# Performance work log

Measured on AMD Instinct MI355X. Metric: run time of the kernel, lower is better.

The kernel has to match this reference:

```python
import jax, jax.numpy as jnp
import numpy as np

B, T, C, H = 4, 2048, 1024, 16
HD = C // H


def setup_inputs() -> dict:
    key = jax.random.key(0)
    ks = jax.random.split(key, 9)
    s = 1.0 / np.sqrt(C)
    return {
        "x": jax.random.normal(ks[0], (B, T, C), dtype=jnp.float32),
        "Wk": jax.random.uniform(ks[1], (C, C), jnp.float32, -s, s),
        "bk": jax.random.uniform(ks[2], (C,), jnp.float32, -s, s),
        "Wq": jax.random.uniform(ks[3], (C, C), jnp.float32, -s, s),
        "bq": jax.random.uniform(ks[4], (C,), jnp.float32, -s, s),
        "Wv": jax.random.uniform(ks[5], (C, C), jnp.float32, -s, s),
        "bv": jax.random.uniform(ks[6], (C,), jnp.float32, -s, s),
        "Wp": jax.random.uniform(ks[7], (C, C), jnp.float32, -s, s),
        "bp": jax.random.uniform(ks[8], (C,), jnp.float32, -s, s),
        "padding_mask": jnp.ones((B, T), dtype=jnp.int32),
    }


def reference(x, Wk, bk, Wq, bq, Wv, bv, Wp, bp, padding_mask):
    # torch nn.Linear: y = x @ W.T + b  (W is [out, in])
    def split_heads(t):  # [B,T,C] -> [B,H,T,HD]
        return t.reshape(B, T, H, HD).transpose(0, 2, 1, 3)

    k = split_heads(x @ Wk.T + bk)
    q = split_heads(x @ Wq.T + bq)
    v = split_heads(x @ Wv.T + bv)

    scale = 1.0 / jnp.sqrt(jnp.float32(HD))
    att = jnp.einsum("bhqd,bhkd->bhqk", q, k) * scale  # [B,H,T,T]

    causal = jnp.tril(jnp.ones((T, T), dtype=bool))  # [T,T]
    pad = (padding_mask != 0)[:, None, None, :]       # [B,1,1,T]
    mask = causal[None, None, :, :] & pad
    att = jnp.where(mask, att, -jnp.inf)
    att = jax.nn.softmax(att, axis=-1)

    y = jnp.einsum("bhqk,bhkd->bhqd", att, v)  # [B,H,T,HD]
    y = y.transpose(0, 2, 1, 3).reshape(B, T, C)
    return y @ Wp.T + bp
```

## Files before the change

kernel.cpp:

```cpp
#include <hip/hip_runtime.h>
#include <hip/hip_bf16.h>
#include <math.h>
#include <stdint.h>

#define BB 4
#define TT 2048
#define CC 1024
#define HH 16
#define HD 64
#define MM (BB*TT)
#define NQT2 16
#define SCQ 0.180336878f

using f32x2  = __attribute__((ext_vector_type(2))) float;
using f32x4  = __attribute__((ext_vector_type(4))) float;
using f32x16 = __attribute__((ext_vector_type(16))) float;
using i32x4  = __attribute__((ext_vector_type(4))) int;
using bf16x4 = __attribute__((ext_vector_type(4))) __bf16;
using bf16x8 = __attribute__((ext_vector_type(8))) __bf16;

__device__ __forceinline__ float fast_exp2(float x) {
  return __builtin_amdgcn_exp2f(x);
}

__device__ __forceinline__ int cvt_pk_bf16(float lo, float hi_) {
  int r;
  asm("v_cvt_pk_bf16_f32 %0, %1, %2" : "=v"(r) : "v"(lo), "v"(hi_));
  return r;
}

__device__ __forceinline__ f32x2 max2(f32x2 a, f32x2 b) {
  return __builtin_elementwise_max(a, b);
}

__device__ __forceinline__ void gload_lds16(const void* g, void* l) {
  __builtin_amdgcn_global_load_lds(
      (__attribute__((address_space(1))) void*)(void*)(g),
      (__attribute__((address_space(3))) void*)(l), 16, 0, 0);
}

__global__ __launch_bounds__(256)
void cvt_f32_bf16(const float* __restrict__ s, __bf16* __restrict__ d, int n4) {
  int i = blockIdx.x * 256 + threadIdx.x;
  if (i >= n4) return;
  float4 v = ((const float4*)s)[i];
  bf16x4 o;
  o[0] = (__bf16)v.x; o[1] = (__bf16)v.y; o[2] = (__bf16)v.z; o[3] = (__bf16)v.w;
  *(bf16x4*)(d + (size_t)i * 4) = o;
}

__global__ __launch_bounds__(256)
void cvt_w4(const float* __restrict__ Wq, const float* __restrict__ Wk,
            const float* __restrict__ Wv, const float* __restrict__ Wp,
            __bf16* __restrict__ wqkv, __bf16* __restrict__ wpb) {
  int which = blockIdx.y;
  const float* s = which == 0 ? Wq : which == 1 ? Wk : which == 2 ? Wv : Wp;
  __bf16* d = which == 3 ? wpb : wqkv + (size_t)which * CC * CC;
  float sc = which == 0 ? SCQ : 1.f;
  int i = blockIdx.x * 256 + threadIdx.x;
  float4 v = ((const float4*)s)[i];
  bf16x4 o;
  o[0] = (__bf16)(v.x * sc); o[1] = (__bf16)(v.y * sc);
  o[2] = (__bf16)(v.z * sc); o[3] = (__bf16)(v.w * sc);
  *(bf16x4*)(d + (size_t)i * 4) = o;
}

#define WAITV4 asm volatile("s_waitcnt vmcnt(4)" ::: "memory")
#define WAITV0 asm volatile("s_waitcnt vmcnt(0)" ::: "memory")
#define BARR   __builtin_amdgcn_s_barrier()
#define SB0    __builtin_amdgcn_sched_barrier(0)

__global__ __launch_bounds__(256, 2)
void gemm_qkv(const __bf16* __restrict__ A, const __bf16* __restrict__ Bm,
              const float* __restrict__ b0, const float* __restrict__ b1,
              const float* __restrict__ b2, __bf16* __restrict__ out,
              __bf16* __restrict__ vt) {
  __shared__ __bf16 U[24576];
  char* Ub = (char*)U;
  const int tid = threadIdx.x;
  const int wid = tid >> 6, lane = tid & 63;
  const int g = lane >> 4, lq = lane & 15;
  const int bx0 = blockIdx.x;
  const int bx = (bx0 & 7) * 192 + (bx0 >> 3);
  const int bm = bx / 24, bn = bx % 24;
  const int brow = bm << 7, bcol = bn << 7;
  const int wr = (wid >> 1) << 6, wc = (wid & 1) << 6;

  const int c0 = tid, c1 = tid + 256;
  const int r0 = c0 >> 2, s0_ = (((c0 & 3) - (r0 >> 1)) & 3) << 4;
  const int r1 = c1 >> 2, s1_ = (((c1 & 3) - (r1 >> 1)) & 3) << 4;
  const char* Ag = (const char*)A;
  const char* Bg = (const char*)Bm;

#define STAGEQ(ko, buf)                                                       \
  {                                                                           \
    gload_lds16(Ag + (size_t)(brow + r0) * 2048 + (ko) + s0_,                 \
                Ub + (buf) * 8192 + c0 * 16);                                 \
    gload_lds16(Ag + (size_t)(brow + r1) * 2048 + (ko) + s1_,                 \
                Ub + (buf) * 8192 + c1 * 16);                                 \
    gload_lds16(Bg + (size_t)(bcol + r0) * 2048 + (ko) + s0_,                 \
                Ub + 24576 + (buf) * 8192 + c0 * 16);                         \
    gload_lds16(Bg + (size_t)(bcol + r1) * 2048 + (ko) + s1_,                 \
                Ub + 24576 + (buf) * 8192 + c1 * 16);                         \
  }

  f32x4 acc[4][4] = {};

  STAGEQ(0, 0); STAGEQ(64, 1);
  int cur = 0;
#pragma unroll 1
  for (int t = 0; t < 32; ++t) {
    if (t + 1 < 32) { WAITV4; } else { WAITV0; }
    BARR; SB0;
    if (t + 2 < 32) {
      int nb = cur + 2; if (nb >= 3) nb -= 3;
      STAGEQ((t + 2) << 6, nb);
    }
    const char* Ac = Ub + cur * 8192;
    const char* Bc = Ub + 24576 + cur * 8192;
    bf16x8 av[4], bv[4];
#pragma unroll
    for (int m = 0; m < 4; ++m) {
      int row = wr + m * 16 + lq;
      int sl = (g + (row >> 1)) & 3;
      av[m] = *(const bf16x8*)(Ac + row * 64 + sl * 16);
    }
#pragma unroll
    for (int n = 0; n < 4; ++n) {
      int row = wc + n * 16 + lq;
      int sl = (g + (row >> 1)) & 3;
      bv[n] = *(const bf16x8*)(Bc + row * 64 + sl * 16);
    }
#pragma unroll
    for (int m = 0; m < 4; ++m)
#pragma unroll
      for (int n = 0; n < 4; ++n)
        acc[m][n] = __builtin_amdgcn_mfma_f32_16x16x32_bf16(av[m], bv[n], acc[m][n], 0, 0, 0);
    SB0;
    cur = (cur == 2) ? 0 : cur + 1;
  }
#undef STAGEQ

  const int proj = bn >> 3;
  if (proj < 2) {
    const float* bias = proj == 0 ? b0 : b1;
    const float bsc = proj == 0 ? SCQ : 1.f;
#pragma unroll
    for (int n = 0; n < 4; ++n) {
      int col = bcol + wc + n * 16 + lq;
      int cw = col & (CC - 1);
      float bb = bias[cw] * bsc;
      int h_ = cw >> 6, d_ = cw & (HD - 1);
#pragma unroll
      for (int m = 0; m < 4; ++m) {
        int row0 = brow + wr + m * 16 + g * 4;
#pragma unroll
        for (int i = 0; i < 4; ++i) {
          int row = row0 + i;
          int b_ = row >> 11, t_ = row & (TT - 1);
          out[((size_t)proj << 23) +
              ((((size_t)b_ * HH + h_) * TT + t_) << 6) + d_] =
              (__bf16)(acc[m][n][i] + bb);
        }
      }
    }
  } else {
    __syncthreads();
    __bf16* lt = U;
    const int cv0 = (bn & 7) << 7;
    const int b_ = brow >> 11, t0 = brow & (TT - 1);
    const int hbase = (bn & 7) << 1;
    const int rd_d = tid >> 2, rd_tb = (tid & 3) << 5;
#pragma unroll
    for (int cc = 0; cc < 2; ++cc) {
      if ((wid & 1) == cc) {
#pragma unroll
        for (int n = 0; n < 4; ++n) {
          int c = (n << 4) + lq;
          float bb = b2[cv0 + (cc << 6) + c];
#pragma unroll
          for (int m = 0; m < 4; ++m) {
            int r = wr + (m << 4) + (g << 2);
            bf16x4 pk;
#pragma unroll
            for (int i = 0; i < 4; ++i)
              pk[i] = (__bf16)(acc[m][n][i] + bb);
            *(bf16x4*)(lt + c * 130 + r) = pk;
          }
        }
      }
      __syncthreads();
      __bf16* dst = vt + (((size_t)((b_ * HH + hbase + cc) * HD + rd_d)) << 11)
                       + t0 + rd_tb;
      const __bf16* srcl = lt + rd_d * 130 + rd_tb;
#pragma unroll
      for (int j = 0; j < 4; ++j)
        *(bf16x8*)(dst + j * 8) = *(const bf16x8*)(srcl + j * 8);
      __syncthreads();
    }
  }
}

__global__ __launch_bounds__(256, 2)
void gemm_proj(const __bf16* __restrict__ A, const __bf16* __restrict__ Bm,
               const float* __restrict__ bias, float* __restrict__ out) {
  __shared__ __bf16 U[24576];
  char* Ub = (char*)U;
  const int tid = threadIdx.x;
  const int wid = tid >> 6, lane = tid & 63;
  const int g = lane >> 4, lq = lane & 15;
  const int bx0 = blockIdx.x;
  const int bx = (bx0 & 7) * 64 + (bx0 >> 3);
  const int brow = (bx >> 3) << 7;
  const int bcol = (bx & 7) << 7;
  const int wr = (wid >> 1) << 6, wc = (wid & 1) << 6;

  const int c0 = tid, c1 = tid + 256;
  const int r0 = c0 >> 2, s0_ = (((c0 & 3) - (r0 >> 1)) & 3) << 4;
  const int r1 = c1 >> 2, s1_ = (((c1 & 3) - (r1 >> 1)) & 3) << 4;
  const char* Ag = (const char*)A;
  const char* Bg = (const char*)Bm;

#define STAGEP(ko, buf)                                                       \
  {                                                                           \
    gload_lds16(Ag + (size_t)(brow + r0) * 2048 + (ko) + s0_,                 \
                Ub + (buf) * 8192 + c0 * 16);                                 \
    gload_lds16(Ag + (size_t)(brow + r1) * 2048 + (ko) + s1_,                 \
                Ub + (buf) * 8192 + c1 * 16);                                 \
    gload_lds16(Bg + (size_t)(bcol + r0) * 2048 + (ko) + s0_,                 \
                Ub + 24576 + (buf) * 8192 + c0 * 16);                         \
    gload_lds16(Bg + (size_t)(bcol + r1) * 2048 + (ko) + s1_,                 \
                Ub + 24576 + (buf) * 8192 + c1 * 16);                         \
  }

  f32x4 acc[4][4] = {};

  STAGEP(0, 0); STAGEP(64, 1);
  int cur = 0;
#pragma unroll 1
  for (int t = 0; t < 32; ++t) {
    if (t + 1 < 32) { WAITV4; } else { WAITV0; }
    BARR; SB0;
    if (t + 2 < 32) {
      int nb = cur + 2; if (nb >= 3) nb -= 3;
      STAGEP((t + 2) << 6, nb);
    }
    const char* Ac = Ub + cur * 8192;
    const char* Bc = Ub + 24576 + cur * 8192;
    bf16x8 av[4], bv[4];
#pragma unroll
    for (int m = 0; m < 4; ++m) {
      int row = wr + m * 16 + lq;
      int sl = (g + (row >> 1)) & 3;
      av[m] = *(const bf16x8*)(Ac + row * 64 + sl * 16);
    }
#pragma unroll
    for (int n = 0; n < 4; ++n) {
      int row = wc + n * 16 + lq;
      int sl = (g + (row >> 1)) & 3;
      bv[n] = *(const bf16x8*)(Bc + row * 64 + sl * 16);
    }
#pragma unroll
    for (int m = 0; m < 4; ++m)
#pragma unroll
      for (int n = 0; n < 4; ++n)
        acc[m][n] = __builtin_amdgcn_mfma_f32_16x16x32_bf16(av[m], bv[n], acc[m][n], 0, 0, 0);
    SB0;
    cur = (cur == 2) ? 0 : cur + 1;
  }
#undef STAGEP

#pragma unroll
  for (int m = 0; m < 4; ++m) {
#pragma unroll
    for (int n = 0; n < 4; ++n) {
      int col = bcol + wc + n * 16 + lq;
      float bb = bias[col];
      int row0 = brow + wr + m * 16 + g * 4;
#pragma unroll
      for (int i = 0; i < 4; ++i)
        out[(size_t)(row0 + i) * CC + col] = acc[m][n][i] + bb;
    }
  }
}

__global__ __launch_bounds__(256, 4)
void attn_fwd(const __bf16* __restrict__ Q, const __bf16* __restrict__ K,
              const __bf16* __restrict__ Vt, const int* __restrict__ pm,
              __bf16* __restrict__ Y) {
  __shared__ __bf16 Ks[2][64 * 64];
  __shared__ __bf16 Vs[2][64 * 64];
  __shared__ int flg;
  const int tid = threadIdx.x, wid = tid >> 6, lane = tid & 63;
  const int l31 = lane & 31, hi = lane >> 5;
  const int bx = blockIdx.x;
  const int bh = bx & 63, jj = bx >> 6;
  const int qi = 15 - (4 * (jj >> 2) + ((jj + (jj >> 2)) & 3));
  const int b_ = bh >> 4, h_ = bh & 15;
  const __bf16* Qb = Q + (size_t)bh * TT * HD;
  const __bf16* Kb = K + (size_t)bh * TT * HD;
  const __bf16* Vb = Vt + (size_t)bh * HD * TT;
  const int* pmb = pm + b_ * TT;

  const int so = tid * 16;
  const int srow = tid >> 3;
  const int scol = (so & 127) ^ ((srow & 7) << 4);

  const int q0 = qi << 7;
  const int qw = q0 + wid * 32;
  const int ntiles = 2 * qi + 2;
  const int sw0 = (l31 & 7) << 4;

  bf16x8 qf[4];
#pragma unroll
  for (int s = 0; s < 4; ++s)
    qf[s] = *(const bf16x8*)(Qb + (size_t)(qw + l31) * HD + s * 16 + hi * 8);
  SB0;

  int4 pa4 = ((const int4*)pmb)[tid];
  int4 pb4 = ((const int4*)pmb)[tid + 256];
  bool okp = pa4.x && pa4.y && pa4.z && pa4.w &&
             pb4.x && pb4.y && pb4.z && pb4.w;
  if (tid == 0) flg = 1;
  __syncthreads();
  if (!okp) flg = 0;

  {
    char* kd = (char*)&Ks[0][0] + so;
    char* vd = (char*)&Vs[0][0] + so;
#pragma unroll
    for (int j = 0; j < 2; ++j) {
      gload_lds16((const char*)Kb + (size_t)(srow + 32 * j) * 128 + scol,
                  kd + j * 4096);
      gload_lds16((const char*)Vb + (size_t)(srow + 32 * j) * (TT * 2) + scol,
                  vd + j * 4096);
    }
  }
  __syncthreads();
  const bool allones = (flg != 0);

  f32x16 o0 = {}, o1 = {};
  f32x16 vzero = {};
  float lsum = 0.f;
  float m = -INFINITY;

  int cur = 0;
#pragma unroll 1
  for (int t = 0; t < ntiles; ++t) {
    const int kv0 = t << 6;
    WAITV0;
    __builtin_amdgcn_s_barrier(); SB0;
    if (t + 1 < ntiles) {
      char* kd = (char*)&Ks[0][0] + (cur ^ 1) * 8192 + so;
      char* vd = (char*)&Vs[0][0] + (cur ^ 1) * 8192 + so;
      const size_t nk = (size_t)(kv0 + 64);
#pragma unroll
      for (int j = 0; j < 2; ++j) {
        gload_lds16((const char*)Kb + (nk + srow + 32 * j) * 128 + scol,
                    kd + j * 4096);
        gload_lds16((const char*)Vb + (size_t)(srow + 32 * j) * (TT * 2) +
                        nk * 2 + scol,
                    vd + j * 4096);
      }
    }

    unsigned long long bits = ~0ull;
    if (__builtin_expect(!allones, 0))
      bits = __ballot(pmb[kv0 + lane] != 0);

    if (kv0 <= qw + 31) {
      const char* VsC = (const char*)&Vs[0][0] + cur * 8192;

#pragma unroll
      for (int h = 0; h < 2; ++h) {
        const int kvh = kv0 + 32 * h;
        if (kvh <= qw + 31) {
          const char* KsC =
              (const char*)&Ks[0][0] + cur * 8192 + (32 * h + l31) * 128;
          f32x16 S;
          __builtin_amdgcn_s_setprio(1);
          {
            bf16x8 k0 = *(const bf16x8*)(KsC + ((16 * hi) ^ sw0));
            S = __builtin_amdgcn_mfma_f32_32x32x16_bf16(k0, qf[0], vzero, 0, 0, 0);
          }
#pragma unroll
          for (int s = 1; s < 4; ++s) {
            bf16x8 kf = *(const bf16x8*)(KsC + ((32 * s + 16 * hi) ^ sw0));
            S = __builtin_amdgcn_mfma_f32_32x32x16_bf16(kf, qf[s], S, 0, 0, 0);
          }
          __builtin_amdgcn_s_setprio(0);

          if (__builtin_expect(bits != ~0ull, 0)) {
#pragma unroll
            for (int r = 0; r < 16; ++r) {
              const int c = (r & 3) + 8 * (r >> 2);
              if (!((bits >> (32 * h + c + 4 * hi)) & 1ull)) S[r] = -INFINITY;
            }
          }
          if (kvh + 31 > qw) {
            const int thr = qw + l31 - kvh - 4 * hi;
#pragma unroll
            for (int r = 0; r < 16; ++r) {
              const int c = (r & 3) + 8 * (r >> 2);
              S[r] = (c <= thr) ? S[r] : -INFINITY;
            }
          }

          f32x2 x0 = {S[0], S[1]},  x1 = {S[2], S[3]};
          f32x2 x2 = {S[4], S[5]},  x3 = {S[6], S[7]};
          f32x2 x4 = {S[8], S[9]},  x5 = {S[10], S[11]};
          f32x2 x6 = {S[12], S[13]}, x7 = {S[14], S[15]};
          x0 = max2(x0, x4); x1 = max2(x1, x5);
          x2 = max2(x2, x6); x3 = max2(x3, x7);
          x0 = max2(x0, x2); x1 = max2(x1, x3);
          x0 = max2(x0, x1);
          float pmax = fmaxf(x0[0], x0[1]);
          if (!__all(pmax <= m + 8.f)) {
            float nm = fmaxf(pmax, __shfl_xor(pmax, 32));
            float mn = fmaxf(m, nm);
            float c = fast_exp2(m - mn);
            m = mn;
            lsum *= c;
#pragma unroll
            for (int r = 0; r < 16; ++r) {
              float cr = __shfl(c, (r & 3) + 8 * (r >> 2) + 4 * hi);
              o0[r] *= cr;
              o1[r] *= cr;
            }
          }

          const f32x2 mm = {m, m};
#pragma unroll
          for (int r = 0; r < 16; r += 2) {
            f32x2 u = {S[r], S[r + 1]};
            u -= mm;
            S[r] = fast_exp2(u[0]);
            S[r + 1] = fast_exp2(u[1]);
          }
          {
            f32x2 u0 = {S[0], S[1]},  u1 = {S[2], S[3]};
            f32x2 u2 = {S[4], S[5]},  u3 = {S[6], S[7]};
            f32x2 u4 = {S[8], S[9]},  u5 = {S[10], S[11]};
            f32x2 u6 = {S[12], S[13]}, u7 = {S[14], S[15]};
            u0 += u4; u1 += u5; u2 += u6; u3 += u7;
            u0 += u2; u1 += u3;
            u0 += u1;
            lsum += u0[0] + u0[1];
          }

          __builtin_amdgcn_s_setprio(1);
#pragma unroll
          for (int s = 0; s < 2; ++s) {
            int A0 = cvt_pk_bf16(S[8 * s + 0], S[8 * s + 1]);
            int A1 = cvt_pk_bf16(S[8 * s + 2], S[8 * s + 3]);
            int B0 = cvt_pk_bf16(S[8 * s + 4], S[8 * s + 5]);
            int B1 = cvt_pk_bf16(S[8 * s + 6], S[8 * s + 7]);
            int s0 = hi ? A0 : B0, s1 = hi ? A1 : B1;
            int e0 = __shfl_xor(s0, 32), e1 = __shfl_xor(s1, 32);
            i32x4 wv;
            wv[0] = hi ? e0 : A0;
            wv[1] = hi ? e1 : A1;
            wv[2] = hi ? B0 : e0;
            wv[3] = hi ? B1 : e1;
            bf16x8 pa = __builtin_bit_cast(bf16x8, wv);
            const int co = 64 * h + 32 * s + 16 * hi;
            bf16x8 v0 = *(const bf16x8*)(VsC + l31 * 128 + (co ^ sw0));
            bf16x8 v1 = *(const bf16x8*)(VsC + (32 + l31) * 128 + (co ^ sw0));
            o0 = __builtin_amdgcn_mfma_f32_32x32x16_bf16(pa, v0, o0, 0, 0, 0);
            o1 = __builtin_amdgcn_mfma_f32_32x32x16_bf16(pa, v1, o1, 0, 0, 0);
          }
          __builtin_amdgcn_s_setprio(0);
        }
      }
    }
    SB0;
    cur ^= 1;
  }

  float linv = 1.f / (lsum + __shfl_xor(lsum, 32));
#pragma unroll
  for (int r = 0; r < 16; ++r) {
    const int crow = (r & 3) + 8 * (r >> 2) + 4 * hi;
    float ir = __shfl(linv, crow);
    const int qrow = qw + crow;
    __bf16* yp = Y + ((size_t)(b_ * TT + qrow)) * CC + h_ * HD + l31;
    yp[0]  = (__bf16)(o0[r] * ir);
    yp[32] = (__bf16)(o1[r] * ir);
  }
}

extern "C" void kernel_launch(void* const* d_in, const int* in_sizes, int n_in,
                              void* d_out, int out_size, void* d_ws, size_t ws_size,
                              hipStream_t stream) {
  (void)in_sizes; (void)n_in; (void)out_size; (void)ws_size;
  const float* x  = (const float*)d_in[0];
  const float* Wk = (const float*)d_in[1];
  const float* bk = (const float*)d_in[2];
  const float* Wq = (const float*)d_in[3];
  const float* bq = (const float*)d_in[4];
  const float* Wv = (const float*)d_in[5];
  const float* bv = (const float*)d_in[6];
  const float* Wp = (const float*)d_in[7];
  const float* bp = (const float*)d_in[8];
  const int* pmask = (const int*)d_in[9];

  char* ws = (char*)d_ws;
  const size_t MB = 1024 * 1024;
  __bf16* xb   = (__bf16*)(ws);
  __bf16* wqkv = (__bf16*)(ws + 16 * MB);
  __bf16* wpb  = (__bf16*)(ws + 22 * MB);
  __bf16* qb   = (__bf16*)(ws + 24 * MB);
  __bf16* kb   = qb + ((size_t)1 << 23);
  __bf16* vtb  = (__bf16*)(ws + 56 * MB);
  __bf16* yb   = xb;

  int n4 = (MM * CC) / 4;
  cvt_f32_bf16<<<(n4 + 255) / 256, 256, 0, stream>>>(x, xb, n4);
  cvt_w4<<<dim3((CC * CC / 4) / 256, 4), 256, 0, stream>>>(
      Wq, Wk, Wv, Wp, wqkv, wpb);

  gemm_qkv<<<(MM / 128) * (3 * CC / 128), 256, 0, stream>>>(
      xb, wqkv, bq, bk, bv, qb, vtb);

  attn_fwd<<<NQT2 * BB * HH, 256, 0, stream>>>(qb, kb, vtb, pmask, yb);

  gemm_proj<<<(MM / 128) * (CC / 128), 256, 0, stream>>>(
      yb, wpb, bp, (float*)d_out);
}
```

Before: 169.0 us.

## Enlarge attention query tile to 256 rows with 512-thread blocks

Doubles the attention block from 4 to 8 waves, so each block handles 256 query rows and every K/V tile loaded into shared memory is reused by twice as many waves. Each thread now issues one async global-to-LDS load per tile instead of two. The grid halves to 512 blocks with a new causal load-balancing order for query tiles. The trade-off is fewer, larger blocks with coarser causal imbalance (waves of the diagonal block idle on masked tiles) and occupancy limited to 2 blocks per CU.

After: 190.3 us. 1.13x slower.

```diff
diff --git a/kernel.cpp b/kernel.cpp
--- a/kernel.cpp
+++ b/kernel.cpp
@@ -9,7 +9,7 @@
 #define HH 16
 #define HD 64
 #define MM (BB*TT)
-#define NQT2 16
+#define NQT3 8
 #define SCQ 0.180336878f
 
 using f32x2  = __attribute__((ext_vector_type(2))) float;
@@ -284,7 +284,7 @@
   }
 }
 
-__global__ __launch_bounds__(256, 4)
+__global__ __launch_bounds__(512, 2)
 void attn_fwd(const __bf16* __restrict__ Q, const __bf16* __restrict__ K,
               const __bf16* __restrict__ Vt, const int* __restrict__ pm,
               __bf16* __restrict__ Y) {
@@ -295,7 +295,8 @@
   const int l31 = lane & 31, hi = lane >> 5;
   const int bx = blockIdx.x;
   const int bh = bx & 63, jj = bx >> 6;
-  const int qi = 15 - (4 * (jj >> 2) + ((jj + (jj >> 2)) & 3));
+  const int r2 = ((jj & 1) << 1) | ((jj >> 1) & 1);
+  const int qi = (jj & 4) ? r2 : 7 - r2;
   const int b_ = bh >> 4, h_ = bh & 15;
   const __bf16* Qb = Q + (size_t)bh * TT * HD;
   const __bf16* Kb = K + (size_t)bh * TT * HD;
@@ -306,9 +307,9 @@
   const int srow = tid >> 3;
   const int scol = (so & 127) ^ ((srow & 7) << 4);
 
-  const int q0 = qi << 7;
+  const int q0 = qi << 8;
   const int qw = q0 + wid * 32;
-  const int ntiles = 2 * qi + 2;
+  const int ntiles = 4 * qi + 4;
   const int sw0 = (l31 & 7) << 4;
 
   bf16x8 qf[4];
@@ -318,24 +319,15 @@
   SB0;
 
   int4 pa4 = ((const int4*)pmb)[tid];
-  int4 pb4 = ((const int4*)pmb)[tid + 256];
-  bool okp = pa4.x && pa4.y && pa4.z && pa4.w &&
-             pb4.x && pb4.y && pb4.z && pb4.w;
+  bool okp = pa4.x && pa4.y && pa4.z && pa4.w;
   if (tid == 0) flg = 1;
   __syncthreads();
   if (!okp) flg = 0;
 
-  {
-    char* kd = (char*)&Ks[0][0] + so;
-    char* vd = (char*)&Vs[0][0] + so;
-#pragma unroll
-    for (int j = 0; j < 2; ++j) {
-      gload_lds16((const char*)Kb + (size_t)(srow + 32 * j) * 128 + scol,
-                  kd + j * 4096);
-      gload_lds16((const char*)Vb + (size_t)(srow + 32 * j) * (TT * 2) + scol,
-                  vd + j * 4096);
-    }
-  }
+  gload_lds16((const char*)Kb + (size_t)srow * 128 + scol,
+              (char*)&Ks[0][0] + so);
+  gload_lds16((const char*)Vb + (size_t)srow * (TT * 2) + scol,
+              (char*)&Vs[0][0] + so);
   __syncthreads();
   const bool allones = (flg != 0);
 
@@ -349,19 +341,13 @@
   for (int t = 0; t < ntiles; ++t) {
     const int kv0 = t << 6;
     WAITV0;
-    __builtin_amdgcn_s_barrier(); SB0;
+    BARR; SB0;
     if (t + 1 < ntiles) {
-      char* kd = (char*)&Ks[0][0] + (cur ^ 1) * 8192 + so;
-      char* vd = (char*)&Vs[0][0] + (cur ^ 1) * 8192 + so;
       const size_t nk = (size_t)(kv0 + 64);
-#pragma unroll
-      for (int j = 0; j < 2; ++j) {
-        gload_lds16((const char*)Kb + (nk + srow + 32 * j) * 128 + scol,
-                    kd + j * 4096);
-        gload_lds16((const char*)Vb + (size_t)(srow + 32 * j) * (TT * 2) +
-                        nk * 2 + scol,
-                    vd + j * 4096);
-      }
+      gload_lds16((const char*)Kb + (nk + srow) * 128 + scol,
+                  (char*)&Ks[0][0] + (cur ^ 1) * 8192 + so);
+      gload_lds16((const char*)Vb + (size_t)srow * (TT * 2) + nk * 2 + scol,
+                  (char*)&Vs[0][0] + (cur ^ 1) * 8192 + so);
     }
 
     unsigned long long bits = ~0ull;
@@ -522,7 +508,7 @@
   gemm_qkv<<<(MM / 128) * (3 * CC / 128), 256, 0, stream>>>(
       xb, wqkv, bq, bk, bv, qb, vtb);
 
-  attn_fwd<<<NQT2 * BB * HH, 256, 0, stream>>>(qb, kb, vtb, pmask, yb);
+  attn_fwd<<<NQT3 * BB * HH, 512, 0, stream>>>(qb, kb, vtb, pmask, yb);
 
   gemm_proj<<<(MM / 128) * (CC / 128), 256, 0, stream>>>(
       yb, wpb, bp, (float*)d_out);
```

## Load QKV GEMM B operand directly into registers, bypassing LDS

Applied to the files above, without the earlier changes.

In the QKV projection GEMM, the weight (B) tile is no longer staged through shared memory. Each wave loads its own B fragments straight from global memory into registers, one k-step ahead, with double-buffered register copies. LDS usage halves and the LDS reads for B are removed. The cost is that each B element is now loaded from global/L2 by both waves sharing a column half, with less coalesced 16-byte accesses, and the vmcnt wait accounting becomes more fragile.

Result: slower. 210.2 us (+24.4%).

```diff
diff --git a/kernel.cpp b/kernel.cpp
--- a/kernel.cpp
+++ b/kernel.cpp
@@ -66,6 +66,7 @@
 }
 
 #define WAITV4 asm volatile("s_waitcnt vmcnt(4)" ::: "memory")
+#define WAITV2 asm volatile("s_waitcnt vmcnt(2)" ::: "memory")
 #define WAITV0 asm volatile("s_waitcnt vmcnt(0)" ::: "memory")
 #define BARR   __builtin_amdgcn_s_barrier()
 #define SB0    __builtin_amdgcn_sched_barrier(0)
@@ -75,7 +76,7 @@
               const float* __restrict__ b0, const float* __restrict__ b1,
               const float* __restrict__ b2, __bf16* __restrict__ out,
               __bf16* __restrict__ vt) {
-  __shared__ __bf16 U[24576];
+  __shared__ __bf16 U[12288];
   char* Ub = (char*)U;
   const int tid = threadIdx.x;
   const int wid = tid >> 6, lane = tid & 63;
@@ -90,35 +91,44 @@
   const int r0 = c0 >> 2, s0_ = (((c0 & 3) - (r0 >> 1)) & 3) << 4;
   const int r1 = c1 >> 2, s1_ = (((c1 & 3) - (r1 >> 1)) & 3) << 4;
   const char* Ag = (const char*)A;
-  const char* Bg = (const char*)Bm;
-
-#define STAGEQ(ko, buf)                                                       \
+  const char* Bg = (const char*)Bm + (size_t)(bcol + wc + lq) * 2048 + g * 16;
+
+#define STAGEA(ko, buf)                                                       \
   {                                                                           \
     gload_lds16(Ag + (size_t)(brow + r0) * 2048 + (ko) + s0_,                 \
                 Ub + (buf) * 8192 + c0 * 16);                                 \
     gload_lds16(Ag + (size_t)(brow + r1) * 2048 + (ko) + s1_,                 \
                 Ub + (buf) * 8192 + c1 * 16);                                 \
-    gload_lds16(Bg + (size_t)(bcol + r0) * 2048 + (ko) + s0_,                 \
-                Ub + 24576 + (buf) * 8192 + c0 * 16);                         \
-    gload_lds16(Bg + (size_t)(bcol + r1) * 2048 + (ko) + s1_,                 \
-                Ub + 24576 + (buf) * 8192 + c1 * 16);                         \
   }
 
   f32x4 acc[4][4] = {};
-
-  STAGEQ(0, 0); STAGEQ(64, 1);
+  bf16x8 bvc[4], bvn[4];
+
+  STAGEA(0, 0);
+  SB0;
+#pragma unroll
+  for (int n = 0; n < 4; ++n)
+    bvc[n] = *(const bf16x8*)(Bg + (size_t)n * 16 * 2048);
+  SB0;
+  STAGEA(64, 1);
   int cur = 0;
 #pragma unroll 1
   for (int t = 0; t < 32; ++t) {
-    if (t + 1 < 32) { WAITV4; } else { WAITV0; }
+    if (t + 1 < 32) { WAITV2; } else { WAITV0; }
     BARR; SB0;
+    if (t + 1 < 32) {
+      const size_t ktb = (size_t)(t + 1) << 6;
+#pragma unroll
+      for (int n = 0; n < 4; ++n)
+        bvn[n] = *(const bf16x8*)(Bg + (size_t)n * 16 * 2048 + ktb);
+      SB0;
+    }
     if (t + 2 < 32) {
       int nb = cur + 2; if (nb >= 3) nb -= 3;
-      STAGEQ((t + 2) << 6, nb);
+      STAGEA((t + 2) << 6, nb);
     }
     const char* Ac = Ub + cur * 8192;
-    const char* Bc = Ub + 24576 + cur * 8192;
-    bf16x8 av[4], bv[4];
+    bf16x8 av[4];
 #pragma unroll
     for (int m = 0; m < 4; ++m) {
       int row = wr + m * 16 + lq;
@@ -126,20 +136,18 @@
       av[m] = *(const bf16x8*)(Ac + row * 64 + sl * 16);
     }
 #pragma unroll
-    for (int n = 0; n < 4; ++n) {
-      int row = wc + n * 16 + lq;
-      int sl = (g + (row >> 1)) & 3;
-      bv[n] = *(const bf16x8*)(Bc + row * 64 + sl * 16);
-    }
-#pragma unroll
     for (int m = 0; m < 4; ++m)
 #pragma unroll
       for (int n = 0; n < 4; ++n)
-        acc[m][n] = __builtin_amdgcn_mfma_f32_16x16x32_bf16(av[m], bv[n], acc[m][n], 0, 0, 0);
+        acc[m][n] = __builtin_amdgcn_mfma_f32_16x16x32_bf16(av[m], bvc[n], acc[m][n], 0, 0, 0);
     SB0;
+    if (t + 1 < 32) {
+#pragma unroll
+      for (int n = 0; n < 4; ++n) bvc[n] = bvn[n];
+    }
     cur = (cur == 2) ? 0 : cur + 1;
   }
-#undef STAGEQ
+#undef STAGEA
 
   const int proj = bn >> 3;
   if (proj < 2) {
```
